# Performance work log

Hardware: AMD Instinct MI355X
Metric: run time of the kernel (lower is better)

## Reference

```python
import jax, jax.numpy as jnp
import numpy as np

DIM = 1024
N_HEADS = 16
HEAD_DIM = DIM // N_HEADS


def setup_inputs() -> dict:
    key = jax.random.key(0)
    kx, kq, kk, kv, ko = jax.random.split(key, 5)
    B, S = 2, 2048
    scale = 1.0 / np.sqrt(DIM)
    return {
        "x": jax.random.normal(kx, (B, S, DIM), dtype=jnp.float32),
        "Wq": jax.random.normal(kq, (DIM, DIM), dtype=jnp.float32) * scale,
        "Wk": jax.random.normal(kk, (DIM, DIM), dtype=jnp.float32) * scale,
        "Wv": jax.random.normal(kv, (DIM, DIM), dtype=jnp.float32) * scale,
        "Wo": jax.random.normal(ko, (DIM, DIM), dtype=jnp.float32) * scale,
    }


def rotate_half(x):
    x1, x2 = jnp.split(x, 2, axis=-1)
    return jnp.concatenate([-x2, x1], axis=-1)


def rope_freqs(seq_len, dim):
    inv_freq = 1.0 / (10000.0 ** (jnp.arange(0, dim, 2, dtype=jnp.float32) / dim))
    t = jnp.arange(seq_len, dtype=jnp.float32)
    freqs = jnp.einsum('i,j->ij', t, inv_freq)  # [S, dim/2]
    return jnp.concatenate([freqs, freqs], axis=-1)  # [S, dim]


def apply_rotary(x, freqs):
    # x: [B, H, S, Dh], freqs: [S, Dh]
    cos = jnp.cos(freqs)[None, None]
    sin = jnp.sin(freqs)[None, None]
    return x * cos + rotate_half(x) * sin


def reference(x, Wq, Wk, Wv, Wo):
    B, S, D = x.shape
    H, Dh = N_HEADS, HEAD_DIM
    # nn.Linear(dim, dim, bias=False): y = x @ W.T
    q = (x @ Wq.T).reshape(B, S, H, Dh).transpose(0, 2, 1, 3)
    k = (x @ Wk.T).reshape(B, S, H, Dh).transpose(0, 2, 1, 3)
    v = (x @ Wv.T).reshape(B, S, H, Dh).transpose(0, 2, 1, 3)
    freqs = rope_freqs(S, Dh)
    q = apply_rotary(q, freqs)
    k = apply_rotary(k, freqs)
    attn = jnp.einsum('bhqd,bhkd->bhqk', q, k) / jnp.sqrt(jnp.float32(Dh))
    attn = jax.nn.softmax(attn, axis=-1)
    out = jnp.einsum('bhqk,bhkd->bhqd', attn, v)
    out = out.transpose(0, 2, 1, 3).reshape(B, S, D)
    return out @ Wo.T
```

## Files before the change

kernel.cpp:

```cpp
#include <hip/hip_runtime.h>
#include <hip/hip_bf16.h>

#define NB 2
#define NS 2048
#define ND 1024
#define NH 16
#define NDH 64
#define NM 4096

typedef __bf16 bf16;
typedef __bf16 bf16x8 __attribute__((ext_vector_type(8)));
typedef __bf16 bf16x4 __attribute__((ext_vector_type(4)));
typedef float f32x4 __attribute__((ext_vector_type(4)));
typedef float f32x16 __attribute__((ext_vector_type(16)));

#define ASYNC16(g, l) __builtin_amdgcn_global_load_lds( \
    (const __attribute__((address_space(1))) void*)(g), \
    (__attribute__((address_space(3))) void*)(l), 16, 0, 0)

static __device__ __forceinline__ unsigned cvt_pk_bf16(float a, float b) {
  unsigned r;
  asm("v_cvt_pk_bf16_f32 %0, %1, %2" : "=v"(r) : "v"(a), "v"(b));
  return r;
}

__global__ __launch_bounds__(256) void convert_kernel(
    const float* __restrict__ x,
    const float* __restrict__ wq, const float* __restrict__ wk,
    const float* __restrict__ wv, const float* __restrict__ wo,
    bf16* __restrict__ xb, bf16* __restrict__ wb) {
  int i = blockIdx.x * 256 + threadIdx.x;
  const int n_x4 = (NM * ND) / 4;
  const int n_w4 = (ND * ND) / 4;
  float4 v;
  bf16* dst;
  if (i < n_x4) {
    v = ((const float4*)x)[i];
    dst = xb + (size_t)i * 4;
  } else {
    int j = i - n_x4;
    int w = j / n_w4;
    int o = j - w * n_w4;
    const float* W = (w == 0) ? wq : (w == 1) ? wk : (w == 2) ? wv : wo;
    v = ((const float4*)W)[o];
    dst = wb + (size_t)w * (ND * ND) + (size_t)o * 4;
  }
  bf16x4 o4;
  o4[0] = (bf16)v.x; o4[1] = (bf16)v.y; o4[2] = (bf16)v.z; o4[3] = (bf16)v.w;
  *(bf16x4*)dst = o4;
}

__global__ __launch_bounds__(256) void tab_kernel(float2* __restrict__ tab) {
  int t = blockIdx.x * 256 + threadIdx.x;
  int s = t >> 5, d = t & 31;
  float invf = exp2f(-0.4152410118609203f * (float)d);
  float f = (float)s * invf;
  float sn, cs;
  sincosf(f, &sn, &cs);
  tab[t] = make_float2(cs, sn);
}

__global__ __launch_bounds__(256) void gemm_qkv(
    const bf16* __restrict__ A, const bf16* __restrict__ Bmat,
    bf16* __restrict__ Qr, bf16* __restrict__ Kr, bf16* __restrict__ vraw,
    const float2* __restrict__ tab) {
  __shared__ bf16 As[128 * 64];
  __shared__ bf16 Bs[128 * 64];
  const int t = threadIdx.x;
  const int lane = t & 63, w = t >> 6;
  const int wr = w >> 1, wc = w & 1;
  const int bm = blockIdx.y * 128;
  const int bn = blockIdx.x * 128;
  const int z = blockIdx.z;
  const bf16* Bz = Bmat + (size_t)z * ND * ND;

  f32x4 acc[4][4];
#pragma unroll
  for (int i = 0; i < 4; ++i)
#pragma unroll
    for (int j = 0; j < 4; ++j) acc[i][j] = (f32x4){0.f, 0.f, 0.f, 0.f};

  for (int kt = 0; kt < ND / 64; ++kt) {
    __syncthreads();
#pragma unroll
    for (int i = 0; i < 4; ++i) {
      int c = w * 64 + lane + i * 256;
      int row = c >> 3;
      int js = (c & 7) ^ (row & 7);
      ASYNC16(A + (size_t)(bm + row) * ND + kt * 64 + js * 8, As + c * 8);
      ASYNC16(Bz + (size_t)(bn + row) * ND + kt * 64 + js * 8, Bs + c * 8);
    }
    __syncthreads();
#pragma unroll
    for (int ks = 0; ks < 2; ++ks) {
      const int kb = ks * 64 + (lane >> 4) * 16;
      bf16x8 af[4], bfr[4];
#pragma unroll
      for (int i = 0; i < 4; ++i) {
        int ra = wr * 64 + i * 16 + (lane & 15);
        af[i] = *(const bf16x8*)((const char*)As + ra * 128 + (kb ^ ((ra & 7) << 4)));
        int rb = wc * 64 + i * 16 + (lane & 15);
        bfr[i] = *(const bf16x8*)((const char*)Bs + rb * 128 + (kb ^ ((rb & 7) << 4)));
      }
#pragma unroll
      for (int i = 0; i < 4; ++i)
#pragma unroll
        for (int j = 0; j < 4; ++j)
          acc[i][j] = __builtin_amdgcn_mfma_f32_16x16x32_bf16(af[i], bfr[j], acc[i][j], 0, 0, 0);
    }
  }

  const int row0 = bm + wr * 64;
  const int col0 = bn + wc * 64;
  if (z == 2) {
#pragma unroll
    for (int i = 0; i < 4; ++i)
#pragma unroll
      for (int j = 0; j < 4; ++j) {
        int r = row0 + i * 16 + (lane >> 4) * 4;
        int ccol = col0 + j * 16 + (lane & 15);
#pragma unroll
        for (int q = 0; q < 4; ++q)
          vraw[(size_t)(r + q) * ND + ccol] = (bf16)acc[i][j][q];
      }
  } else {
    bf16* dst = z ? Kr : Qr;
    const float qs = z ? 1.0f : 0.1803368801111204f;
    const int h = col0 >> 6;
    const int ln15 = lane & 15;
#pragma unroll
    for (int i = 0; i < 4; ++i)
#pragma unroll
      for (int j = 0; j < 2; ++j)
#pragma unroll
        for (int q = 0; q < 4; ++q) {
          int r = row0 + i * 16 + (lane >> 4) * 4 + q;
          int b = r >> 11, s = r & (NS - 1);
          int d1 = j * 16 + ln15;
          float2 tc = tab[s * 32 + d1];
          float x1 = acc[i][j][q], x2 = acc[i][j + 2][q];
          size_t base = ((size_t)((b * NH + h) * NS + s)) * NDH;
          dst[base + d1]      = (bf16)((x1 * tc.x - x2 * tc.y) * qs);
          dst[base + d1 + 32] = (bf16)((x2 * tc.x + x1 * tc.y) * qs);
        }
  }
}

__global__ __launch_bounds__(256) void gemm_out(
    const bf16* __restrict__ A, const bf16* __restrict__ Bmat,
    float* __restrict__ Cout) {
  __shared__ bf16 As[128 * 64];
  __shared__ bf16 Bs[64 * 64];
  const int t = threadIdx.x;
  const int lane = t & 63, w = t >> 6;
  const int wr = w >> 1, wc = w & 1;
  const int bm = blockIdx.y * 128;
  const int bn = blockIdx.x * 64;

  f32x4 acc[4][2];
#pragma unroll
  for (int i = 0; i < 4; ++i)
#pragma unroll
    for (int j = 0; j < 2; ++j) acc[i][j] = (f32x4){0.f, 0.f, 0.f, 0.f};

  for (int kt = 0; kt < ND / 64; ++kt) {
    __syncthreads();
#pragma unroll
    for (int i = 0; i < 4; ++i) {
      int c = i * 256 + t;
      int row = c >> 3;
      int js = (c & 7) ^ (row & 7);
      ASYNC16(A + (size_t)(bm + row) * ND + kt * 64 + js * 8, As + c * 8);
    }
#pragma unroll
    for (int i = 0; i < 2; ++i) {
      int c = i * 256 + t;
      int row = c >> 3;
      int js = (c & 7) ^ (row & 7);
      ASYNC16(Bmat + (size_t)(bn + row) * ND + kt * 64 + js * 8, Bs + c * 8);
    }
    __syncthreads();
#pragma unroll
    for (int ks = 0; ks < 2; ++ks) {
      const int kb = ks * 64 + (lane >> 4) * 16;
      bf16x8 af[4], bfr[2];
#pragma unroll
      for (int i = 0; i < 4; ++i) {
        int ra = wr * 64 + i * 16 + (lane & 15);
        af[i] = *(const bf16x8*)((const char*)As + ra * 128 + (kb ^ ((ra & 7) << 4)));
      }
#pragma unroll
      for (int j = 0; j < 2; ++j) {
        int rb = wc * 32 + j * 16 + (lane & 15);
        bfr[j] = *(const bf16x8*)((const char*)Bs + rb * 128 + (kb ^ ((rb & 7) << 4)));
      }
#pragma unroll
      for (int i = 0; i < 4; ++i)
#pragma unroll
        for (int j = 0; j < 2; ++j)
          acc[i][j] = __builtin_amdgcn_mfma_f32_16x16x32_bf16(af[i], bfr[j], acc[i][j], 0, 0, 0);
    }
  }

  const int row0 = bm + wr * 64;
  const int col0 = bn + wc * 32;
#pragma unroll
  for (int i = 0; i < 4; ++i)
#pragma unroll
    for (int j = 0; j < 2; ++j) {
      int r = row0 + i * 16 + (lane >> 4) * 4;
      int ccol = col0 + j * 16 + (lane & 15);
#pragma unroll
      for (int q = 0; q < 4; ++q)
        Cout[(size_t)(r + q) * ND + ccol] = acc[i][j][q];
    }
}

__global__ __launch_bounds__(256) void transv_kernel(
    const bf16* __restrict__ vraw, bf16* __restrict__ VT) {
  __shared__ bf16 tl[64][65];
  int s0 = blockIdx.x * 64;
  int bh = blockIdx.y;
  int b = bh >> 4, h = bh & 15;
  int t = threadIdx.x;
#pragma unroll
  for (int i = 0; i < 4; ++i) {
    int row = (t >> 4) + i * 16;
    int d4 = (t & 15) * 4;
    *(bf16x4*)&tl[row][d4] =
        *(const bf16x4*)&vraw[((size_t)(b * NS + s0 + row)) * ND + h * NDH + d4];
  }
  __syncthreads();
#pragma unroll
  for (int i = 0; i < 4; ++i) {
    int dr = (t >> 4) + i * 16;
    int s4 = (t & 15) * 4;
    bf16x4 o;
    o[0] = tl[s4 + 0][dr]; o[1] = tl[s4 + 1][dr];
    o[2] = tl[s4 + 2][dr]; o[3] = tl[s4 + 3][dr];
    *(bf16x4*)&VT[((size_t)(bh * NDH + dr)) * NS + s0 + s4] = o;
  }
}

__global__ __launch_bounds__(256, 2) void attn_kernel(
    const bf16* __restrict__ Qr, const bf16* __restrict__ Kr,
    const bf16* __restrict__ VT, bf16* __restrict__ out) {
  __shared__ bf16 Ks[2][512 * 8];
  __shared__ bf16 Vs[2][512 * 8];
  const int t = threadIdx.x, lane = t & 63, w = t >> 6;
  const int hi = lane >> 5, ln = lane & 31;
  int wg = blockIdx.x;
  int sw = (wg & 7) * 64 + (wg >> 3);
  const int qb = sw & 15, bh = sw >> 4;
  const int q0 = qb * 128 + w * 32;

  bf16x8 qv[4];
  {
    const bf16* Qb = Qr + ((size_t)bh * NS + q0 + ln) * NDH + hi * 8;
#pragma unroll
    for (int c = 0; c < 4; ++c) qv[c] = *(const bf16x8*)(Qb + c * 16);
  }

  f32x16 O0, O1;
#pragma unroll
  for (int r = 0; r < 16; ++r) { O0[r] = 0.f; O1[r] = 0.f; }
  float m = -1e30f, l = 0.f;

#define STAGE_KV(nb, kt2)                                                     \
  {                                                                           \
    _Pragma("unroll")                                                         \
    for (int i = 0; i < 2; ++i) {                                             \
      int ch = i * 256 + t;                                                   \
      int cp = ch >> 6, row = ch & 63;                                        \
      ASYNC16(Kr + ((size_t)bh * NS + (kt2) * 64 + row) * NDH + cp * 8,       \
              &Ks[nb][0] + ch * 8);                                           \
      ASYNC16(VT + ((size_t)bh * NDH + row) * NS + (kt2) * 64 + cp * 8,       \
              &Vs[nb][0] + ch * 8);                                           \
    }                                                                         \
  }

  STAGE_KV(0, 0);
  __syncthreads();

  int cur = 0;
  for (int kt = 0; kt < NS / 64; ++kt) {
    if (kt + 1 < NS / 64) STAGE_KV(cur ^ 1, kt + 1);
    const bf16* Kb = &Ks[cur][0];
    const bf16* Vb = &Vs[cur][0];

    f32x16 s0, s1;
#pragma unroll
    for (int r = 0; r < 16; ++r) { s0[r] = 0.f; s1[r] = 0.f; }
    bf16x8 k0[4], k1[4];
#pragma unroll
    for (int c = 0; c < 4; ++c) {
      k0[c] = *(const bf16x8*)(Kb + (2 * c + hi) * 512 + ln * 8);
      k1[c] = *(const bf16x8*)(Kb + (2 * c + hi) * 512 + (32 + ln) * 8);
    }
    __builtin_amdgcn_s_setprio(1);
#pragma unroll
    for (int c = 0; c < 4; ++c) {
      s0 = __builtin_amdgcn_mfma_f32_32x32x16_bf16(k0[c], qv[c], s0, 0, 0, 0);
      s1 = __builtin_amdgcn_mfma_f32_32x32x16_bf16(k1[c], qv[c], s1, 0, 0, 0);
    }
    __builtin_amdgcn_s_setprio(0);

    float a0[8];
#pragma unroll
    for (int r = 0; r < 8; ++r) a0[r] = fmaxf(fmaxf(s0[r], s0[r + 8]), fmaxf(s1[r], s1[r + 8]));
    float b0 = fmaxf(fmaxf(a0[0], a0[1]), fmaxf(a0[2], a0[3]));
    float b1 = fmaxf(fmaxf(a0[4], a0[5]), fmaxf(a0[6], a0[7]));
    float pmax = fmaxf(b0, b1);
    pmax = fmaxf(pmax, __shfl_xor(pmax, 32, 64));

    if (!__all(pmax - m <= 8.0f)) {
      float mnew = fmaxf(m, pmax);
      float scl = exp2f(m - mnew);
      m = mnew; l *= scl;
#pragma unroll
      for (int r = 0; r < 16; ++r) { O0[r] *= scl; O1[r] *= scl; }
    }

    float p0[16], p1[16];
#pragma unroll
    for (int r = 0; r < 16; ++r) { p0[r] = exp2f(s0[r] - m); p1[r] = exp2f(s1[r] - m); }
    float sp[8];
#pragma unroll
    for (int r = 0; r < 8; ++r) sp[r] = (p0[r] + p0[r + 8]) + (p1[r] + p1[r + 8]);
    float sum = (((sp[0] + sp[1]) + (sp[2] + sp[3])) + ((sp[4] + sp[5]) + (sp[6] + sp[7])));
    sum += __shfl_xor(sum, 32, 64);
    l += sum;

    unsigned u0[8], u1[8], x0[8], x1[8];
#pragma unroll
    for (int g = 0; g < 4; ++g) {
      u0[g]     = cvt_pk_bf16(p0[4 * g],     p0[4 * g + 1]);
      u1[g]     = cvt_pk_bf16(p0[4 * g + 2], p0[4 * g + 3]);
      u0[4 + g] = cvt_pk_bf16(p1[4 * g],     p1[4 * g + 1]);
      u1[4 + g] = cvt_pk_bf16(p1[4 * g + 2], p1[4 * g + 3]);
    }
#pragma unroll
    for (int g = 0; g < 8; ++g) {
      x0[g] = __shfl_xor(u0[g], 32, 64);
      x1[g] = __shfl_xor(u1[g], 32, 64);
    }

    bf16x8 v0[4], v1[4];
#pragma unroll
    for (int c = 0; c < 4; ++c) {
      v0[c] = *(const bf16x8*)(Vb + (2 * c + hi) * 512 + ln * 8);
      v1[c] = *(const bf16x8*)(Vb + (2 * c + hi) * 512 + (32 + ln) * 8);
    }
    __builtin_amdgcn_s_setprio(1);
#pragma unroll
    for (int c = 0; c < 4; ++c) {
      int base = (c >> 1) * 4 + (c & 1) * 2;
      union { unsigned u[4]; bf16x8 v; } pa;
      pa.u[0] = hi ? x0[base + 1] : u0[base];
      pa.u[1] = hi ? x1[base + 1] : u1[base];
      pa.u[2] = hi ? u0[base + 1] : x0[base];
      pa.u[3] = hi ? u1[base + 1] : x1[base];
      O0 = __builtin_amdgcn_mfma_f32_32x32x16_bf16(pa.v, v0[c], O0, 0, 0, 0);
      O1 = __builtin_amdgcn_mfma_f32_32x32x16_bf16(pa.v, v1[c], O1, 0, 0, 0);
    }
    __builtin_amdgcn_s_setprio(0);

    __syncthreads();
    cur ^= 1;
  }

  float rl = 1.0f / l;
  const int b = bh >> 4, h = bh & 15;
#pragma unroll
  for (int r = 0; r < 16; ++r) {
    int q = (r & 3) + 8 * (r >> 2) + 4 * hi;
    float rlq = __shfl(rl, q, 64);
    int s = q0 + q;
    size_t base = ((size_t)(b * NS + s)) * ND + h * NDH + ln;
    out[base]      = (bf16)(O0[r] * rlq);
    out[base + 32] = (bf16)(O1[r] * rlq);
  }
}

extern "C" void kernel_launch(void* const* d_in, const int* in_sizes, int n_in,
                              void* d_out, int out_size, void* d_ws, size_t ws_size,
                              hipStream_t stream) {
  const float* x  = (const float*)d_in[0];
  const float* wq = (const float*)d_in[1];
  const float* wk = (const float*)d_in[2];
  const float* wv = (const float*)d_in[3];
  const float* wo = (const float*)d_in[4];
  char* ws = (char*)d_ws;
  bf16* xb    = (bf16*)(ws);
  bf16* wb    = (bf16*)(ws + (8u << 20));
  bf16* vraw  = (bf16*)(ws + (16u << 20));
  bf16* Qr    = (bf16*)(ws + (24u << 20));
  bf16* Kr    = (bf16*)(ws + (32u << 20));
  bf16* VT    = (bf16*)(ws + (40u << 20));
  bf16* attnb = (bf16*)(ws + (48u << 20));
  float2* tab = (float2*)(ws + (56u << 20));
  float* out  = (float*)d_out;

  convert_kernel<<<8192, 256, 0, stream>>>(x, wq, wk, wv, wo, xb, wb);
  tab_kernel<<<256, 256, 0, stream>>>(tab);
  gemm_qkv<<<dim3(8, 32, 3), 256, 0, stream>>>(xb, wb, Qr, Kr, vraw, tab);
  transv_kernel<<<dim3(32, 32), 256, 0, stream>>>(vraw, VT);
  attn_kernel<<<dim3(512), 256, 0, stream>>>(Qr, Kr, VT, attnb);
  gemm_out<<<dim3(16, 32), 256, 0, stream>>>(attnb, wb + 3 * ND * ND, out);
}
```

Measured before the change: 224.4 us.

## Pre-tile K and V in global memory so attention stages contiguous 8KB blocks

K and transposed V are now written by the producer kernels in a tiled layout that matches the attention kernel's shared-memory staging order. Each 64-key tile becomes one contiguous 8KB block, so the async global-to-LDS loads read sequential addresses instead of strided rows. The cost is scattered 2-byte stores in the QKV GEMM epilogue for K, and 8-byte strided stores in the V transpose.

```diff
diff --git a/kernel.cpp b/kernel.cpp
--- a/kernel.cpp
+++ b/kernel.cpp
@@ -7,6 +7,8 @@
 #define NH 16
 #define NDH 64
 #define NM 4096
+#define KVT 4096
+#define KVBH (NS * NDH)
 
 typedef __bf16 bf16;
 typedef __bf16 bf16x8 __attribute__((ext_vector_type(8)));
@@ -62,7 +64,7 @@
 
 __global__ __launch_bounds__(256) void gemm_qkv(
     const bf16* __restrict__ A, const bf16* __restrict__ Bmat,
-    bf16* __restrict__ Qr, bf16* __restrict__ Kr, bf16* __restrict__ vraw,
+    bf16* __restrict__ Qr, bf16* __restrict__ Kg, bf16* __restrict__ vraw,
     const float2* __restrict__ tab) {
   __shared__ bf16 As[128 * 64];
   __shared__ bf16 Bs[128 * 64];
@@ -124,7 +126,6 @@
           vraw[(size_t)(r + q) * ND + ccol] = (bf16)acc[i][j][q];
       }
   } else {
-    bf16* dst = z ? Kr : Qr;
     const float qs = z ? 1.0f : 0.1803368801111204f;
     const int h = col0 >> 6;
     const int ln15 = lane & 15;
@@ -139,9 +140,18 @@
           int d1 = j * 16 + ln15;
           float2 tc = tab[s * 32 + d1];
           float x1 = acc[i][j][q], x2 = acc[i][j + 2][q];
-          size_t base = ((size_t)((b * NH + h) * NS + s)) * NDH;
-          dst[base + d1]      = (bf16)((x1 * tc.x - x2 * tc.y) * qs);
-          dst[base + d1 + 32] = (bf16)((x2 * tc.x + x1 * tc.y) * qs);
+          float y1 = (x1 * tc.x - x2 * tc.y) * qs;
+          float y2 = (x2 * tc.x + x1 * tc.y) * qs;
+          if (z == 0) {
+            size_t base = ((size_t)((b * NH + h) * NS + s)) * NDH;
+            Qr[base + d1]      = (bf16)y1;
+            Qr[base + d1 + 32] = (bf16)y2;
+          } else {
+            size_t kb2 = ((size_t)(b * NH + h)) * KVBH + (size_t)(s >> 6) * KVT + (s & 63) * 8;
+            int cp1 = d1 >> 3, e1 = d1 & 7;
+            Kg[kb2 + cp1 * 512 + e1]       = (bf16)y1;
+            Kg[kb2 + (cp1 + 4) * 512 + e1] = (bf16)y2;
+          }
         }
   }
 }
@@ -217,7 +227,7 @@
 }
 
 __global__ __launch_bounds__(256) void transv_kernel(
-    const bf16* __restrict__ vraw, bf16* __restrict__ VT) {
+    const bf16* __restrict__ vraw, bf16* __restrict__ Vg) {
   __shared__ bf16 tl[64][65];
   int s0 = blockIdx.x * 64;
   int bh = blockIdx.y;
@@ -231,6 +241,7 @@
         *(const bf16x4*)&vraw[((size_t)(b * NS + s0 + row)) * ND + h * NDH + d4];
   }
   __syncthreads();
+  const size_t tbase = (size_t)bh * KVBH + (size_t)(s0 >> 6) * KVT;
 #pragma unroll
   for (int i = 0; i < 4; ++i) {
     int dr = (t >> 4) + i * 16;
@@ -238,13 +249,13 @@
     bf16x4 o;
     o[0] = tl[s4 + 0][dr]; o[1] = tl[s4 + 1][dr];
     o[2] = tl[s4 + 2][dr]; o[3] = tl[s4 + 3][dr];
-    *(bf16x4*)&VT[((size_t)(bh * NDH + dr)) * NS + s0 + s4] = o;
+    *(bf16x4*)&Vg[tbase + (s4 >> 3) * 512 + dr * 8 + (s4 & 7)] = o;
   }
 }
 
 __global__ __launch_bounds__(256, 2) void attn_kernel(
-    const bf16* __restrict__ Qr, const bf16* __restrict__ Kr,
-    const bf16* __restrict__ VT, bf16* __restrict__ out) {
+    const bf16* __restrict__ Qr, const bf16* __restrict__ Kg,
+    const bf16* __restrict__ Vg, bf16* __restrict__ out) {
   __shared__ bf16 Ks[2][512 * 8];
   __shared__ bf16 Vs[2][512 * 8];
   const int t = threadIdx.x, lane = t & 63, w = t >> 6;
@@ -253,6 +264,7 @@
   int sw = (wg & 7) * 64 + (wg >> 3);
   const int qb = sw & 15, bh = sw >> 4;
   const int q0 = qb * 128 + w * 32;
+  const size_t kvbase = (size_t)bh * KVBH;
 
   bf16x8 qv[4];
   {
@@ -271,11 +283,8 @@
     _Pragma("unroll")                                                         \
     for (int i = 0; i < 2; ++i) {                                             \
       int ch = i * 256 + t;                                                   \
-      int cp = ch >> 6, row = ch & 63;                                        \
-      ASYNC16(Kr + ((size_t)bh * NS + (kt2) * 64 + row) * NDH + cp * 8,       \
-              &Ks[nb][0] + ch * 8);                                           \
-      ASYNC16(VT + ((size_t)bh * NDH + row) * NS + (kt2) * 64 + cp * 8,       \
-              &Vs[nb][0] + ch * 8);                                           \
+      ASYNC16(Kg + kvbase + (size_t)(kt2) * KVT + ch * 8, &Ks[nb][0] + ch * 8); \
+      ASYNC16(Vg + kvbase + (size_t)(kt2) * KVT + ch * 8, &Vs[nb][0] + ch * 8); \
     }                                                                         \
   }
 
@@ -395,16 +404,16 @@
   bf16* wb    = (bf16*)(ws + (8u << 20));
   bf16* vraw  = (bf16*)(ws + (16u << 20));
   bf16* Qr    = (bf16*)(ws + (24u << 20));
-  bf16* Kr    = (bf16*)(ws + (32u << 20));
-  bf16* VT    = (bf16*)(ws + (40u << 20));
+  bf16* Kg    = (bf16*)(ws + (32u << 20));
+  bf16* Vg    = (bf16*)(ws + (40u << 20));
   bf16* attnb = (bf16*)(ws + (48u << 20));
   float2* tab = (float2*)(ws + (56u << 20));
   float* out  = (float*)d_out;
 
   convert_kernel<<<8192, 256, 0, stream>>>(x, wq, wk, wv, wo, xb, wb);
   tab_kernel<<<256, 256, 0, stream>>>(tab);
-  gemm_qkv<<<dim3(8, 32, 3), 256, 0, stream>>>(xb, wb, Qr, Kr, vraw, tab);
-  transv_kernel<<<dim3(32, 32), 256, 0, stream>>>(vraw, VT);
-  attn_kernel<<<dim3(512), 256, 0, stream>>>(Qr, Kr, VT, attnb);
+  gemm_qkv<<<dim3(8, 32, 3), 256, 0, stream>>>(xb, wb, Qr, Kg, vraw, tab);
+  transv_kernel<<<dim3(32, 32), 256, 0, stream>>>(vraw, Vg);
+  attn_kernel<<<dim3(512), 256, 0, stream>>>(Qr, Kg, Vg, attnb);
   gemm_out<<<dim3(16, 32), 256, 0, stream>>>(attnb, wb + 3 * ND * ND, out);
 }
```

New measurement: 227.9 us. No clear change (+1.5%).
